# Kernel optimization log

Measured on AMD Instinct MI355X. Metric: run time of the kernel, lower is better.

Reference implementation:

```python
import jax, jax.numpy as jnp
import numpy as np

N_ROUTING = 3


def squash(s):
    # squash factor ||s|| / (1 + ||s||^2), applied per output capsule vector
    n = jnp.linalg.norm(s, axis=-1, keepdims=True)
    return n / (1.0 + n * n) * s


def setup_inputs() -> dict:
    key = jax.random.key(0)
    k1, k2 = jax.random.split(key)
    B, Ni, Di = 64, 2048, 8
    No, Do = 32, 16
    x = jax.random.normal(k1, (B, Ni, Di), dtype=jnp.float32)
    W = jax.random.normal(k2, (Ni, No, Do, Di), dtype=jnp.float32) * 0.05
    return {"x": x, "W": W}


def reference(x, W):
    # x: (B, Ni, Di); W: (Ni, No, Do, Di)
    # Per-capsule transform: x_hat[b,i,j,:] = W[i,j] @ x[b,i]
    x_hat = jnp.einsum('bni,nodi->bnod', x, W)          # (B, Ni, No, Do)
    x_hat_sg = jax.lax.stop_gradient(x_hat)
    B, Ni, No, Do = x_hat.shape
    b = jnp.zeros((B, Ni, No), dtype=x_hat.dtype)       # routing logits
    v = None
    for it in range(N_ROUTING):
        c = jax.nn.softmax(b, axis=2)                   # coupling over output caps
        if it == N_ROUTING - 1:
            s = jnp.einsum('bno,bnod->bod', c, x_hat)   # grads flow on last iter
            v = squash(s)
        else:
            s = jnp.einsum('bno,bnod->bod', c, x_hat_sg)
            v = squash(s)
            b = b + jnp.einsum('bod,bnod->bno', v, x_hat_sg)  # agreement update
    return v  # (B, No, Do)
```

## Files before the change

### kernel.cpp

```cpp
#include <hip/hip_runtime.h>
#include <hip/hip_bf16.h>
#include <math.h>

namespace {
constexpr int kB  = 64;
constexpr int kNi = 2048;
constexpr int kNo = 32;
constexpr int kDo = 16;
constexpr int kSeg   = kNo * kDo;
constexpr int kSlabs = 256;
constexpr int kNPer  = kNi / kSlabs;
}

typedef __attribute__((ext_vector_type(4)))  short s4;
typedef __attribute__((ext_vector_type(16))) float f16v;

__device__ __forceinline__ f16v mfma_32x32x8_bf16(s4 a, s4 b, f16v c) {
#if __has_builtin(__builtin_amdgcn_mfma_f32_32x32x8bf16_1k)
    return __builtin_amdgcn_mfma_f32_32x32x8bf16_1k(a, b, c, 0, 0, 0);
#else
    asm("v_mfma_f32_32x32x8_bf16 %0, %1, %2, %0" : "+v"(c) : "v"(a), "v"(b));
    return c;
#endif
}

__device__ __forceinline__ unsigned pack_bf16(float lo, float hi) {
    union { __hip_bfloat162 h; unsigned u; } v;
    v.h = __float22bfloat162_rn(make_float2(lo, hi));
    return v.u;
}
__device__ __forceinline__ float bf_lo(unsigned u) { return __uint_as_float(u << 16); }
__device__ __forceinline__ float bf_hi(unsigned u) { return __uint_as_float(u & 0xffff0000u); }

union A2 { int2 i; s4 s; };

__global__ __launch_bounds__(256, 4)
void caps_prep(const float* __restrict__ xg, const float* __restrict__ Wg,
               unsigned* __restrict__ wPack2, unsigned* __restrict__ xPack)
{
    const int t = blockIdx.x * 256 + threadIdx.x;
    const int nW = kNi * 16 * 64;
    if (t < nW) {
        const int n = t >> 10, rem = t & 1023, mt = rem >> 6, l = rem & 63;
        const float4 w = *reinterpret_cast<const float4*>(
            Wg + ((size_t)n * kSeg + mt * 32 + (l & 31)) * 8 + 4 * (l >> 5));
        const size_t base = (((size_t)n * 8 + (mt >> 1)) * 64 + l) * 4 + (mt & 1) * 2;
        uint2 u; u.x = pack_bf16(w.x, w.y); u.y = pack_bf16(w.z, w.w);
        *reinterpret_cast<uint2*>(wPack2 + base) = u;
    } else {
        const int t2 = t - nW;
        const int n = t2 >> 7, rem = t2 & 127, nt = rem >> 6, l = rem & 63;
        const float4 v = *reinterpret_cast<const float4*>(
            xg + ((size_t)(nt * 32 + (l & 31)) * kNi + n) * 8 + 4 * (l >> 5));
        uint2 u; u.x = pack_bf16(v.x, v.y); u.y = pack_bf16(v.z, v.w);
        *reinterpret_cast<uint2*>(xPack + (size_t)t2 * 2) = u;
    }
}


__global__ __launch_bounds__(512, 2)
void caps_logits(const unsigned* __restrict__ wPack2, const unsigned* __restrict__ xPack,
                 const float* __restrict__ vsumPack, unsigned* __restrict__ cbuf)
{
    __shared__ float Zl[2][8][4][32];

    const int tid = threadIdx.x;
    const int blk = blockIdx.x & (kSlabs - 1);
    const int nt  = blockIdx.x >> 8;
    const int w   = __builtin_amdgcn_readfirstlane(tid >> 6);
    const int l   = tid & 63;
    const int b32 = l & 31;
    const int b   = nt * 32 + b32;
    const int hi  = l >> 5;

    float vsp[2][16];
#pragma unroll
    for (int m = 0; m < 2; ++m) {
        const int mt = 2 * w + m;
        const float4* vp = reinterpret_cast<const float4*>(
            vsumPack + (((size_t)mt * 2 + hi) * 64 + b) * 16);
#pragma unroll
        for (int k = 0; k < 4; ++k) {
            const float4 v = vp[k];
            vsp[m][4 * k + 0] = v.x; vsp[m][4 * k + 1] = v.y;
            vsp[m][4 * k + 2] = v.z; vsp[m][4 * k + 3] = v.w;
        }
    }

    const int4* wp4 = reinterpret_cast<const int4*>(wPack2);
    const int2* xp2 = reinterpret_cast<const int2*>(xPack);
    const size_t abase = ((size_t)blk * 64 + w) * 64 + l;
    const size_t xbase = ((size_t)blk * 16 + nt) * 64 + l;

    for (int h = 0; h < 2; ++h) {
        float e[4][4];
#pragma unroll
        for (int k = 0; k < 4; ++k) {
            const int nn = h * 4 + k;
            const int4 aw = wp4[abase + (size_t)nn * 512];
            const int2 bx = xp2[xbase + (size_t)nn * 128];
            A2 ua0; ua0.i = make_int2(aw.x, aw.y);
            A2 ua1; ua1.i = make_int2(aw.z, aw.w);
            A2 ub;  ub.i  = bx;
            f16v t0, t1;
#pragma unroll
            for (int r = 0; r < 16; ++r) { t0[r] = 0.0f; t1[r] = 0.0f; }
            t0 = mfma_32x32x8_bf16(ua0.s, ub.s, t0);
            t1 = mfma_32x32x8_bf16(ua1.s, ub.s, t1);
            {
                float a0_ = fmaf(vsp[0][1], t0[1], vsp[0][0] * t0[0]);
                float a1_ = fmaf(vsp[0][3], t0[3], vsp[0][2] * t0[2]);
                float a2_ = fmaf(vsp[0][5], t0[5], vsp[0][4] * t0[4]);
                float a3_ = fmaf(vsp[0][7], t0[7], vsp[0][6] * t0[6]);
                float p0 = (a0_ + a1_) + (a2_ + a3_);
                float b0_ = fmaf(vsp[0][9],  t0[9],  vsp[0][8]  * t0[8]);
                float b1_ = fmaf(vsp[0][11], t0[11], vsp[0][10] * t0[10]);
                float b2_ = fmaf(vsp[0][13], t0[13], vsp[0][12] * t0[12]);
                float b3_ = fmaf(vsp[0][15], t0[15], vsp[0][14] * t0[14]);
                float p1 = (b0_ + b1_) + (b2_ + b3_);
                p0 += __shfl_xor(p0, 32);
                p1 += __shfl_xor(p1, 32);
                e[k][0] = exp2f(p0); e[k][1] = exp2f(p1);
            }
            {
                float a0_ = fmaf(vsp[1][1], t1[1], vsp[1][0] * t1[0]);
                float a1_ = fmaf(vsp[1][3], t1[3], vsp[1][2] * t1[2]);
                float a2_ = fmaf(vsp[1][5], t1[5], vsp[1][4] * t1[4]);
                float a3_ = fmaf(vsp[1][7], t1[7], vsp[1][6] * t1[6]);
                float p0 = (a0_ + a1_) + (a2_ + a3_);
                float b0_ = fmaf(vsp[1][9],  t1[9],  vsp[1][8]  * t1[8]);
                float b1_ = fmaf(vsp[1][11], t1[11], vsp[1][10] * t1[10]);
                float b2_ = fmaf(vsp[1][13], t1[13], vsp[1][12] * t1[12]);
                float b3_ = fmaf(vsp[1][15], t1[15], vsp[1][14] * t1[14]);
                float p1 = (b0_ + b1_) + (b2_ + b3_);
                p0 += __shfl_xor(p0, 32);
                p1 += __shfl_xor(p1, 32);
                e[k][2] = exp2f(p0); e[k][3] = exp2f(p1);
            }
            if (l < 32)
                Zl[h][w][k][l] = (e[k][0] + e[k][1]) + (e[k][2] + e[k][3]);
        }
        __syncthreads();
#pragma unroll
        for (int k = 0; k < 4; ++k) {
            float Z = 0.0f;
#pragma unroll
            for (int w2 = 0; w2 < 8; ++w2) Z += Zl[h][w2][k][b32];
            const float rz = __builtin_amdgcn_rcpf(Z);
            if (l < 32) {
                const size_t idx =
                    (((size_t)(blk * 8 + h * 4 + k) * 16) + 2 * w) * 64 + b;
                cbuf[idx]      = pack_bf16(e[k][0] * rz, e[k][1] * rz);
                cbuf[idx + 64] = pack_bf16(e[k][2] * rz, e[k][3] * rz);
            }
        }
    }
}

template<int PASS>
__global__ __launch_bounds__(512, 2)
void caps_accum(const unsigned* __restrict__ wPack2, const unsigned* __restrict__ xPack,
                const unsigned* __restrict__ cbuf, __hip_bfloat16* __restrict__ partial)
{
    const int tid = threadIdx.x;
    const int blk = blockIdx.x & (kSlabs - 1);
    const int nt  = blockIdx.x >> 8;
    const int w   = __builtin_amdgcn_readfirstlane(tid >> 6);
    const int l   = tid & 63;
    const int b32 = l & 31;
    const int b   = nt * 32 + b32;
    const int hi  = l >> 5;

    float sacc[2][16];
    f16v acc0, acc1;
#pragma unroll
    for (int r = 0; r < 16; ++r) {
        sacc[0][r] = 0.0f; sacc[1][r] = 0.0f;
        acc0[r] = 0.0f;    acc1[r] = 0.0f;
    }

    const int4* wp4 = reinterpret_cast<const int4*>(wPack2);
    const int2* xp2 = reinterpret_cast<const int2*>(xPack);
    const size_t abase = ((size_t)blk * 64 + w) * 64 + l;
    const size_t xbase = ((size_t)blk * 16 + nt) * 64 + l;
    const size_t cbase = ((size_t)blk * 128 + 2 * w) * 64 + b;

#pragma unroll 2
    for (int nn = 0; nn < kNPer; ++nn) {
        const int4 aw = wp4[abase + (size_t)nn * 512];
        const int2 bx = xp2[xbase + (size_t)nn * 128];
        A2 ua0; ua0.i = make_int2(aw.x, aw.y);
        A2 ua1; ua1.i = make_int2(aw.z, aw.w);
        A2 ub;  ub.i  = bx;

        if (PASS == 0) {
            acc0 = mfma_32x32x8_bf16(ua0.s, ub.s, acc0);
            acc1 = mfma_32x32x8_bf16(ua1.s, ub.s, acc1);
        } else {
            const unsigned cp0 = cbuf[cbase + (size_t)nn * 1024];
            const unsigned cp1 = cbuf[cbase + (size_t)nn * 1024 + 64];
            f16v t0, t1;
#pragma unroll
            for (int r = 0; r < 16; ++r) { t0[r] = 0.0f; t1[r] = 0.0f; }
            t0 = mfma_32x32x8_bf16(ua0.s, ub.s, t0);
            t1 = mfma_32x32x8_bf16(ua1.s, ub.s, t1);
            const float c00 = bf_lo(cp0), c01 = bf_hi(cp0);
            const float c10 = bf_lo(cp1), c11 = bf_hi(cp1);
#pragma unroll
            for (int r = 0; r < 8; ++r) {
                sacc[0][r]     = fmaf(c00, t0[r],     sacc[0][r]);
                sacc[0][8 + r] = fmaf(c01, t0[8 + r], sacc[0][8 + r]);
                sacc[1][r]     = fmaf(c10, t1[r],     sacc[1][r]);
                sacc[1][8 + r] = fmaf(c11, t1[8 + r], sacc[1][8 + r]);
            }
        }
    }

#pragma unroll
    for (int m = 0; m < 2; ++m) {
        const int mt = 2 * w + m;
#pragma unroll
        for (int q = 0; q < 4; ++q) {
            const int od = mt * 32 + 8 * q + 4 * hi;
            float v0, v1, v2, v3;
            if (PASS == 0) {
                const f16v& a = (m == 0) ? acc0 : acc1;
                v0 = a[4 * q + 0]; v1 = a[4 * q + 1];
                v2 = a[4 * q + 2]; v3 = a[4 * q + 3];
            } else {
                v0 = sacc[m][4 * q + 0]; v1 = sacc[m][4 * q + 1];
                v2 = sacc[m][4 * q + 2]; v3 = sacc[m][4 * q + 3];
            }
            uint2 u; u.x = pack_bf16(v0, v1); u.y = pack_bf16(v2, v3);
            *reinterpret_cast<uint2*>(
                partial + ((size_t)blk * kB + b) * kSeg + od) = u;
        }
    }
}

template<int PASS>
__global__ __launch_bounds__(512, 2)
void caps_finish(const __hip_bfloat16* __restrict__ partial,
                 float* __restrict__ vsum, float* __restrict__ vsumPack,
                 float* __restrict__ out)
{
    const int b  = blockIdx.x >> 2;
    const int q  = blockIdx.x & 3;
    const int t  = threadIdx.x;
    const int tl = t & 127;
    const int cg = t >> 7;
    const int od = q * 128 + tl;

    const __hip_bfloat16* p = partial
        + ((size_t)(cg * 64) * kB + b) * kSeg + od;
    float s = 0.0f;
#pragma unroll 16
    for (int k = 0; k < 64; ++k)
        s += __bfloat162float(p[(size_t)k * (kB * kSeg)]);

    __shared__ float red[4][128];
    __shared__ float sq[128];
    __shared__ float fo[8];
    red[cg][tl] = s;
    __syncthreads();
    if (t < 128) {
        s = (red[0][tl] + red[1][tl]) + (red[2][tl] + red[3][tl]);
        if (PASS == 0) s *= (1.0f / 32.0f);
        sq[tl] = s * s;
    }
    __syncthreads();
    if (t < 8) {
        float n2 = 0.0f;
#pragma unroll
        for (int d = 0; d < 16; ++d) n2 += sq[t * 16 + d];
        fo[t] = sqrtf(n2) / (1.0f + n2);
    }
    __syncthreads();
    if (t < 128) {
        const float v = fo[tl >> 4] * s;
        float nv = v;
        if (PASS == 0) {
            vsum[(size_t)b * kSeg + od] = v;
        } else if (PASS == 1) {
            nv = vsum[(size_t)b * kSeg + od] + v;
            vsum[(size_t)b * kSeg + od] = nv;
        } else {
            out[(size_t)b * kSeg + od] = v;
        }
        if (PASS < 2) {
            const int mt = od >> 5, r5 = od & 31;
            const int hi = (r5 >> 2) & 1, reg = (r5 & 3) | ((r5 >> 3) << 2);
            vsumPack[(((size_t)mt * 2 + hi) * 64 + b) * 16 + reg] =
                nv * 1.44269504f;
        }
    }
}

extern "C" void kernel_launch(void* const* d_in, const int* in_sizes, int n_in,
                              void* d_out, int out_size, void* d_ws, size_t ws_size,
                              hipStream_t stream)
{
    const float* x = (const float*)d_in[0];
    const float* W = (const float*)d_in[1];
    float* out = (float*)d_out;

    char* base = (char*)d_ws;
    __hip_bfloat16* partial = (__hip_bfloat16*)base;
    base += (size_t)kSlabs * kB * kSeg * sizeof(__hip_bfloat16);
    float* vsum = (float*)base;
    base += (size_t)kB * kSeg * sizeof(float);
    float* vsumPack = (float*)base;
    base += (size_t)16 * 2 * 64 * 16 * sizeof(float);
    unsigned* wPack2 = (unsigned*)base;
    base += (size_t)kNi * 16 * 64 * 2 * sizeof(unsigned);
    unsigned* xPack = (unsigned*)base;
    base += (size_t)kNi * 2 * 64 * 4 * sizeof(unsigned);
    unsigned* cbuf = (unsigned*)base;

    caps_prep<<<dim3(9216), dim3(256), 0, stream>>>(x, W, wPack2, xPack);

    const dim3 gr(kSlabs * 2), br(512);
    const dim3 gf(kB * 4), bf(512);

    caps_accum<0><<<gr, br, 0, stream>>>(wPack2, xPack, cbuf, partial);
    caps_finish<0><<<gf, bf, 0, stream>>>(partial, vsum, vsumPack, out);
    caps_logits<<<gr, br, 0, stream>>>(wPack2, xPack, vsumPack, cbuf);
    caps_accum<1><<<gr, br, 0, stream>>>(wPack2, xPack, cbuf, partial);
    caps_finish<1><<<gf, bf, 0, stream>>>(partial, vsum, vsumPack, out);
    caps_logits<<<gr, br, 0, stream>>>(wPack2, xPack, vsumPack, cbuf);
    caps_accum<1><<<gr, br, 0, stream>>>(wPack2, xPack, cbuf, partial);
    caps_finish<2><<<gf, bf, 0, stream>>>(partial, vsum, vsumPack, out);
}
```

Measured before the change: 85.10 us.

## Fuse routing-logit softmax and weighted accumulation into one kernel via LDS coupling buffer

```diff
diff --git a/kernel.cpp b/kernel.cpp
--- a/kernel.cpp
+++ b/kernel.cpp
@@ -59,10 +59,59 @@
 
 
 __global__ __launch_bounds__(512, 2)
-void caps_logits(const unsigned* __restrict__ wPack2, const unsigned* __restrict__ xPack,
-                 const float* __restrict__ vsumPack, unsigned* __restrict__ cbuf)
+void caps_acc0(const unsigned* __restrict__ wPack2, const unsigned* __restrict__ xPack,
+               __hip_bfloat16* __restrict__ partial)
+{
+    const int tid = threadIdx.x;
+    const int blk = blockIdx.x & (kSlabs - 1);
+    const int nt  = blockIdx.x >> 8;
+    const int w   = __builtin_amdgcn_readfirstlane(tid >> 6);
+    const int l   = tid & 63;
+    const int b   = nt * 32 + (l & 31);
+    const int hi  = l >> 5;
+
+    f16v acc0, acc1;
+#pragma unroll
+    for (int r = 0; r < 16; ++r) { acc0[r] = 0.0f; acc1[r] = 0.0f; }
+
+    const int4* wp4 = reinterpret_cast<const int4*>(wPack2);
+    const int2* xp2 = reinterpret_cast<const int2*>(xPack);
+    const size_t abase = ((size_t)blk * 64 + w) * 64 + l;
+    const size_t xbase = ((size_t)blk * 16 + nt) * 64 + l;
+
+#pragma unroll 2
+    for (int nn = 0; nn < kNPer; ++nn) {
+        const int4 aw = wp4[abase + (size_t)nn * 512];
+        const int2 bx = xp2[xbase + (size_t)nn * 128];
+        A2 ua0; ua0.i = make_int2(aw.x, aw.y);
+        A2 ua1; ua1.i = make_int2(aw.z, aw.w);
+        A2 ub;  ub.i  = bx;
+        acc0 = mfma_32x32x8_bf16(ua0.s, ub.s, acc0);
+        acc1 = mfma_32x32x8_bf16(ua1.s, ub.s, acc1);
+    }
+
+#pragma unroll
+    for (int m = 0; m < 2; ++m) {
+        const int mt = 2 * w + m;
+        const f16v& a = (m == 0) ? acc0 : acc1;
+#pragma unroll
+        for (int q = 0; q < 4; ++q) {
+            const int od = mt * 32 + 8 * q + 4 * hi;
+            uint2 u;
+            u.x = pack_bf16(a[4 * q + 0], a[4 * q + 1]);
+            u.y = pack_bf16(a[4 * q + 2], a[4 * q + 3]);
+            *reinterpret_cast<uint2*>(
+                partial + ((size_t)blk * kB + b) * kSeg + od) = u;
+        }
+    }
+}
+
+__global__ __launch_bounds__(512, 2)
+void caps_routef(const unsigned* __restrict__ wPack2, const unsigned* __restrict__ xPack,
+                 const float* __restrict__ vsumPack, __hip_bfloat16* __restrict__ partial)
 {
     __shared__ float Zl[2][8][4][32];
+    __shared__ unsigned cl[kNPer][16][32];
 
     const int tid = threadIdx.x;
     const int blk = blockIdx.x & (kSlabs - 1);
@@ -73,117 +122,94 @@
     const int b   = nt * 32 + b32;
     const int hi  = l >> 5;
 
-    float vsp[2][16];
-#pragma unroll
-    for (int m = 0; m < 2; ++m) {
-        const int mt = 2 * w + m;
-        const float4* vp = reinterpret_cast<const float4*>(
-            vsumPack + (((size_t)mt * 2 + hi) * 64 + b) * 16);
-#pragma unroll
-        for (int k = 0; k < 4; ++k) {
-            const float4 v = vp[k];
-            vsp[m][4 * k + 0] = v.x; vsp[m][4 * k + 1] = v.y;
-            vsp[m][4 * k + 2] = v.z; vsp[m][4 * k + 3] = v.w;
-        }
-    }
-
     const int4* wp4 = reinterpret_cast<const int4*>(wPack2);
     const int2* xp2 = reinterpret_cast<const int2*>(xPack);
     const size_t abase = ((size_t)blk * 64 + w) * 64 + l;
     const size_t xbase = ((size_t)blk * 16 + nt) * 64 + l;
 
-    for (int h = 0; h < 2; ++h) {
-        float e[4][4];
-#pragma unroll
-        for (int k = 0; k < 4; ++k) {
-            const int nn = h * 4 + k;
-            const int4 aw = wp4[abase + (size_t)nn * 512];
-            const int2 bx = xp2[xbase + (size_t)nn * 128];
-            A2 ua0; ua0.i = make_int2(aw.x, aw.y);
-            A2 ua1; ua1.i = make_int2(aw.z, aw.w);
-            A2 ub;  ub.i  = bx;
-            f16v t0, t1;
-#pragma unroll
-            for (int r = 0; r < 16; ++r) { t0[r] = 0.0f; t1[r] = 0.0f; }
-            t0 = mfma_32x32x8_bf16(ua0.s, ub.s, t0);
-            t1 = mfma_32x32x8_bf16(ua1.s, ub.s, t1);
-            {
-                float a0_ = fmaf(vsp[0][1], t0[1], vsp[0][0] * t0[0]);
-                float a1_ = fmaf(vsp[0][3], t0[3], vsp[0][2] * t0[2]);
-                float a2_ = fmaf(vsp[0][5], t0[5], vsp[0][4] * t0[4]);
-                float a3_ = fmaf(vsp[0][7], t0[7], vsp[0][6] * t0[6]);
-                float p0 = (a0_ + a1_) + (a2_ + a3_);
-                float b0_ = fmaf(vsp[0][9],  t0[9],  vsp[0][8]  * t0[8]);
-                float b1_ = fmaf(vsp[0][11], t0[11], vsp[0][10] * t0[10]);
-                float b2_ = fmaf(vsp[0][13], t0[13], vsp[0][12] * t0[12]);
-                float b3_ = fmaf(vsp[0][15], t0[15], vsp[0][14] * t0[14]);
-                float p1 = (b0_ + b1_) + (b2_ + b3_);
-                p0 += __shfl_xor(p0, 32);
-                p1 += __shfl_xor(p1, 32);
-                e[k][0] = exp2f(p0); e[k][1] = exp2f(p1);
+    {
+        float vsp[2][16];
+#pragma unroll
+        for (int m = 0; m < 2; ++m) {
+            const int mt = 2 * w + m;
+            const float4* vp = reinterpret_cast<const float4*>(
+                vsumPack + (((size_t)mt * 2 + hi) * 64 + b) * 16);
+#pragma unroll
+            for (int k = 0; k < 4; ++k) {
+                const float4 v = vp[k];
+                vsp[m][4 * k + 0] = v.x; vsp[m][4 * k + 1] = v.y;
+                vsp[m][4 * k + 2] = v.z; vsp[m][4 * k + 3] = v.w;
             }
-            {
-                float a0_ = fmaf(vsp[1][1], t1[1], vsp[1][0] * t1[0]);
-                float a1_ = fmaf(vsp[1][3], t1[3], vsp[1][2] * t1[2]);
-                float a2_ = fmaf(vsp[1][5], t1[5], vsp[1][4] * t1[4]);
-                float a3_ = fmaf(vsp[1][7], t1[7], vsp[1][6] * t1[6]);
-                float p0 = (a0_ + a1_) + (a2_ + a3_);
-                float b0_ = fmaf(vsp[1][9],  t1[9],  vsp[1][8]  * t1[8]);
-                float b1_ = fmaf(vsp[1][11], t1[11], vsp[1][10] * t1[10]);
-                float b2_ = fmaf(vsp[1][13], t1[13], vsp[1][12] * t1[12]);
-                float b3_ = fmaf(vsp[1][15], t1[15], vsp[1][14] * t1[14]);
-                float p1 = (b0_ + b1_) + (b2_ + b3_);
-                p0 += __shfl_xor(p0, 32);
-                p1 += __shfl_xor(p1, 32);
-                e[k][2] = exp2f(p0); e[k][3] = exp2f(p1);
+        }
+
+        for (int h = 0; h < 2; ++h) {
+            float e[4][4];
+#pragma unroll
+            for (int k = 0; k < 4; ++k) {
+                const int nn = h * 4 + k;
+                const int4 aw = wp4[abase + (size_t)nn * 512];
+                const int2 bx = xp2[xbase + (size_t)nn * 128];
+                A2 ua0; ua0.i = make_int2(aw.x, aw.y);
+                A2 ua1; ua1.i = make_int2(aw.z, aw.w);
+                A2 ub;  ub.i  = bx;
+                f16v t0, t1;
+#pragma unroll
+                for (int r = 0; r < 16; ++r) { t0[r] = 0.0f; t1[r] = 0.0f; }
+                t0 = mfma_32x32x8_bf16(ua0.s, ub.s, t0);
+                t1 = mfma_32x32x8_bf16(ua1.s, ub.s, t1);
+                {
+                    float a0_ = fmaf(vsp[0][1], t0[1], vsp[0][0] * t0[0]);
+                    float a1_ = fmaf(vsp[0][3], t0[3], vsp[0][2] * t0[2]);
+                    float a2_ = fmaf(vsp[0][5], t0[5], vsp[0][4] * t0[4]);
+                    float a3_ = fmaf(vsp[0][7], t0[7], vsp[0][6] * t0[6]);
+                    float p0 = (a0_ + a1_) + (a2_ + a3_);
+                    float b0_ = fmaf(vsp[0][9],  t0[9],  vsp[0][8]  * t0[8]);
+                    float b1_ = fmaf(vsp[0][11], t0[11], vsp[0][10] * t0[10]);
+                    float b2_ = fmaf(vsp[0][13], t0[13], vsp[0][12] * t0[12]);
+                    float b3_ = fmaf(vsp[0][15], t0[15], vsp[0][14] * t0[14]);
+                    float p1 = (b0_ + b1_) + (b2_ + b3_);
+                    p0 += __shfl_xor(p0, 32);
+                    p1 += __shfl_xor(p1, 32);
+                    e[k][0] = exp2f(p0); e[k][1] = exp2f(p1);
+                }
+                {
+                    float a0_ = fmaf(vsp[1][1], t1[1], vsp[1][0] * t1[0]);
+                    float a1_ = fmaf(vsp[1][3], t1[3], vsp[1][2] * t1[2]);
+                    float a2_ = fmaf(vsp[1][5], t1[5], vsp[1][4] * t1[4]);
+                    float a3_ = fmaf(vsp[1][7], t1[7], vsp[1][6] * t1[6]);
+                    float p0 = (a0_ + a1_) + (a2_ + a3_);
+                    float b0_ = fmaf(vsp[1][9],  t1[9],  vsp[1][8]  * t1[8]);
+                    float b1_ = fmaf(vsp[1][11], t1[11], vsp[1][10] * t1[10]);
+                    float b2_ = fmaf(vsp[1][13], t1[13], vsp[1][12] * t1[12]);
+                    float b3_ = fmaf(vsp[1][15], t1[15], vsp[1][14] * t1[14]);
+                    float p1 = (b0_ + b1_) + (b2_ + b3_);
+                    p0 += __shfl_xor(p0, 32);
+                    p1 += __shfl_xor(p1, 32);
+                    e[k][2] = exp2f(p0); e[k][3] = exp2f(p1);
+                }
+                if (l < 32)
+                    Zl[h][w][k][l] = (e[k][0] + e[k][1]) + (e[k][2] + e[k][3]);
             }
-            if (l < 32)
-                Zl[h][w][k][l] = (e[k][0] + e[k][1]) + (e[k][2] + e[k][3]);
-        }
-        __syncthreads();
-#pragma unroll
-        for (int k = 0; k < 4; ++k) {
-            float Z = 0.0f;
-#pragma unroll
-            for (int w2 = 0; w2 < 8; ++w2) Z += Zl[h][w2][k][b32];
-            const float rz = __builtin_amdgcn_rcpf(Z);
-            if (l < 32) {
-                const size_t idx =
-                    (((size_t)(blk * 8 + h * 4 + k) * 16) + 2 * w) * 64 + b;
-                cbuf[idx]      = pack_bf16(e[k][0] * rz, e[k][1] * rz);
-                cbuf[idx + 64] = pack_bf16(e[k][2] * rz, e[k][3] * rz);
+            __syncthreads();
+#pragma unroll
+            for (int k = 0; k < 4; ++k) {
+                float Z = 0.0f;
+#pragma unroll
+                for (int w2 = 0; w2 < 8; ++w2) Z += Zl[h][w2][k][b32];
+                const float rz = __builtin_amdgcn_rcpf(Z);
+                if (l < 32) {
+                    cl[h * 4 + k][2 * w + 0][l] = pack_bf16(e[k][0] * rz, e[k][1] * rz);
+                    cl[h * 4 + k][2 * w + 1][l] = pack_bf16(e[k][2] * rz, e[k][3] * rz);
+                }
             }
         }
     }
-}
-
-template<int PASS>
-__global__ __launch_bounds__(512, 2)
-void caps_accum(const unsigned* __restrict__ wPack2, const unsigned* __restrict__ xPack,
-                const unsigned* __restrict__ cbuf, __hip_bfloat16* __restrict__ partial)
-{
-    const int tid = threadIdx.x;
-    const int blk = blockIdx.x & (kSlabs - 1);
-    const int nt  = blockIdx.x >> 8;
-    const int w   = __builtin_amdgcn_readfirstlane(tid >> 6);
-    const int l   = tid & 63;
-    const int b32 = l & 31;
-    const int b   = nt * 32 + b32;
-    const int hi  = l >> 5;
+    __syncthreads();
+    __builtin_amdgcn_sched_barrier(0);
 
     float sacc[2][16];
-    f16v acc0, acc1;
-#pragma unroll
-    for (int r = 0; r < 16; ++r) {
-        sacc[0][r] = 0.0f; sacc[1][r] = 0.0f;
-        acc0[r] = 0.0f;    acc1[r] = 0.0f;
-    }
-
-    const int4* wp4 = reinterpret_cast<const int4*>(wPack2);
-    const int2* xp2 = reinterpret_cast<const int2*>(xPack);
-    const size_t abase = ((size_t)blk * 64 + w) * 64 + l;
-    const size_t xbase = ((size_t)blk * 16 + nt) * 64 + l;
-    const size_t cbase = ((size_t)blk * 128 + 2 * w) * 64 + b;
+#pragma unroll
+    for (int r = 0; r < 16; ++r) { sacc[0][r] = 0.0f; sacc[1][r] = 0.0f; }
 
 #pragma unroll 2
     for (int nn = 0; nn < kNPer; ++nn) {
@@ -192,27 +218,21 @@
         A2 ua0; ua0.i = make_int2(aw.x, aw.y);
         A2 ua1; ua1.i = make_int2(aw.z, aw.w);
         A2 ub;  ub.i  = bx;
-
-        if (PASS == 0) {
-            acc0 = mfma_32x32x8_bf16(ua0.s, ub.s, acc0);
-            acc1 = mfma_32x32x8_bf16(ua1.s, ub.s, acc1);
-        } else {
-            const unsigned cp0 = cbuf[cbase + (size_t)nn * 1024];
-            const unsigned cp1 = cbuf[cbase + (size_t)nn * 1024 + 64];
-            f16v t0, t1;
-#pragma unroll
-            for (int r = 0; r < 16; ++r) { t0[r] = 0.0f; t1[r] = 0.0f; }
-            t0 = mfma_32x32x8_bf16(ua0.s, ub.s, t0);
-            t1 = mfma_32x32x8_bf16(ua1.s, ub.s, t1);
-            const float c00 = bf_lo(cp0), c01 = bf_hi(cp0);
-            const float c10 = bf_lo(cp1), c11 = bf_hi(cp1);
-#pragma unroll
-            for (int r = 0; r < 8; ++r) {
-                sacc[0][r]     = fmaf(c00, t0[r],     sacc[0][r]);
-                sacc[0][8 + r] = fmaf(c01, t0[8 + r], sacc[0][8 + r]);
-                sacc[1][r]     = fmaf(c10, t1[r],     sacc[1][r]);
-                sacc[1][8 + r] = fmaf(c11, t1[8 + r], sacc[1][8 + r]);
-            }
+        const unsigned cp0 = cl[nn][2 * w + 0][b32];
+        const unsigned cp1 = cl[nn][2 * w + 1][b32];
+        f16v t0, t1;
+#pragma unroll
+        for (int r = 0; r < 16; ++r) { t0[r] = 0.0f; t1[r] = 0.0f; }
+        t0 = mfma_32x32x8_bf16(ua0.s, ub.s, t0);
+        t1 = mfma_32x32x8_bf16(ua1.s, ub.s, t1);
+        const float c00 = bf_lo(cp0), c01 = bf_hi(cp0);
+        const float c10 = bf_lo(cp1), c11 = bf_hi(cp1);
+#pragma unroll
+        for (int r = 0; r < 8; ++r) {
+            sacc[0][r]     = fmaf(c00, t0[r],     sacc[0][r]);
+            sacc[0][8 + r] = fmaf(c01, t0[8 + r], sacc[0][8 + r]);
+            sacc[1][r]     = fmaf(c10, t1[r],     sacc[1][r]);
+            sacc[1][8 + r] = fmaf(c11, t1[8 + r], sacc[1][8 + r]);
         }
     }
 
@@ -222,16 +242,9 @@
 #pragma unroll
         for (int q = 0; q < 4; ++q) {
             const int od = mt * 32 + 8 * q + 4 * hi;
-            float v0, v1, v2, v3;
-            if (PASS == 0) {
-                const f16v& a = (m == 0) ? acc0 : acc1;
-                v0 = a[4 * q + 0]; v1 = a[4 * q + 1];
-                v2 = a[4 * q + 2]; v3 = a[4 * q + 3];
-            } else {
-                v0 = sacc[m][4 * q + 0]; v1 = sacc[m][4 * q + 1];
-                v2 = sacc[m][4 * q + 2]; v3 = sacc[m][4 * q + 3];
-            }
-            uint2 u; u.x = pack_bf16(v0, v1); u.y = pack_bf16(v2, v3);
+            uint2 u;
+            u.x = pack_bf16(sacc[m][4 * q + 0], sacc[m][4 * q + 1]);
+            u.y = pack_bf16(sacc[m][4 * q + 2], sacc[m][4 * q + 3]);
             *reinterpret_cast<uint2*>(
                 partial + ((size_t)blk * kB + b) * kSeg + od) = u;
         }
@@ -314,20 +327,16 @@
     unsigned* wPack2 = (unsigned*)base;
     base += (size_t)kNi * 16 * 64 * 2 * sizeof(unsigned);
     unsigned* xPack = (unsigned*)base;
-    base += (size_t)kNi * 2 * 64 * 4 * sizeof(unsigned);
-    unsigned* cbuf = (unsigned*)base;
 
     caps_prep<<<dim3(9216), dim3(256), 0, stream>>>(x, W, wPack2, xPack);
 
     const dim3 gr(kSlabs * 2), br(512);
     const dim3 gf(kB * 4), bf(512);
 
-    caps_accum<0><<<gr, br, 0, stream>>>(wPack2, xPack, cbuf, partial);
+    caps_acc0<<<gr, br, 0, stream>>>(wPack2, xPack, partial);
     caps_finish<0><<<gf, bf, 0, stream>>>(partial, vsum, vsumPack, out);
-    caps_logits<<<gr, br, 0, stream>>>(wPack2, xPack, vsumPack, cbuf);
-    caps_accum<1><<<gr, br, 0, stream>>>(wPack2, xPack, cbuf, partial);
+    caps_routef<<<gr, br, 0, stream>>>(wPack2, xPack, vsumPack, partial);
     caps_finish<1><<<gf, bf, 0, stream>>>(partial, vsum, vsumPack, out);
-    caps_logits<<<gr, br, 0, stream>>>(wPack2, xPack, vsumPack, cbuf);
-    caps_accum<1><<<gr, br, 0, stream>>>(wPack2, xPack, cbuf, partial);
+    caps_routef<<<gr, br, 0, stream>>>(wPack2, xPack, vsumPack, partial);
     caps_finish<2><<<gf, bf, 0, stream>>>(partial, vsum, vsumPack, out);
 }
```

Measured after the change: 79.41 us. 6.7% less time.
